# Optimization experiments

Hardware: AMD Instinct MI355X
Metric: run time of the kernel (lower is better)

Reference implementation:

```python
import jax, jax.numpy as jnp
import numpy as np

IN_CH = 128
OUT_CH = 1
N_NODES = 20000
N_EDGES = 640000
EPS = 1e-5


def setup_inputs() -> dict:
    key = jax.random.key(0)
    ks = jax.random.split(key, 8)
    x = jax.random.normal(ks[0], (N_NODES, IN_CH), dtype=jnp.float32)
    edge_index = jax.random.randint(ks[1], (2, N_EDGES), 0, N_NODES, dtype=jnp.int64)
    s1 = 1.0 / np.sqrt(2 * IN_CH)
    s2 = 1.0 / np.sqrt(IN_CH)
    return {
        "x": x,
        "edge_index": edge_index,
        "W1": jax.random.normal(ks[2], (2 * IN_CH, IN_CH), dtype=jnp.float32) * s1,
        "b1": jnp.zeros((IN_CH,), dtype=jnp.float32),
        "bn_g": jnp.ones((IN_CH,), dtype=jnp.float32),
        "bn_b": jnp.zeros((IN_CH,), dtype=jnp.float32),
        "W2": jax.random.normal(ks[3], (IN_CH, IN_CH), dtype=jnp.float32) * s2,
        "b2": jnp.zeros((IN_CH,), dtype=jnp.float32),
        "ln_g": jnp.ones((IN_CH,), dtype=jnp.float32),
        "ln_b": jnp.zeros((IN_CH,), dtype=jnp.float32),
        "W3": jax.random.normal(ks[4], (IN_CH, OUT_CH), dtype=jnp.float32) * s2,
        "b3": jnp.zeros((OUT_CH,), dtype=jnp.float32),
    }


def gcn_conv(h, src, dst, num_nodes, bias):
    # h: [num_nodes, F] already linearly transformed. GCN norm with self loops:
    # deg[i] = 1 + in-degree(i); norm_e = deg[src]^-1/2 * deg[dst]^-1/2
    deg = jnp.zeros((num_nodes,), h.dtype).at[dst].add(1.0) + 1.0
    dinv = deg ** -0.5
    norm = dinv[src] * dinv[dst]                      # [E]
    agg = jnp.zeros_like(h).at[dst].add(h[src] * norm[:, None])
    agg = agg + h * (dinv * dinv)[:, None]            # self-loop contribution
    return agg + bias


def reference(x, edge_index, W1, b1, bn_g, bn_b, W2, b2, ln_g, ln_b, W3, b3):
    src, dst = edge_index[0], edge_index[1]
    E = src.shape[0]
    # edge features: [E, 2*IN_CH]
    ef = jnp.concatenate([x[src], x[dst]], axis=1)
    # GCNConv 1 over E "nodes" (edge-feature rows)
    h = gcn_conv(ef @ W1, src, dst, E, b1)
    # BatchNorm1d (training-mode batch stats, biased variance)
    mean = h.mean(axis=0)
    var = h.var(axis=0)
    h = (h - mean) * jax.lax.rsqrt(var + EPS) * bn_g + bn_b
    h = jax.nn.relu(h)
    # GCNConv 2
    h = gcn_conv(h @ W2, src, dst, E, b2)
    # LayerNorm over feature dim
    mu = h.mean(axis=-1, keepdims=True)
    v = h.var(axis=-1, keepdims=True)
    h = (h - mu) * jax.lax.rsqrt(v + EPS) * ln_g + ln_b
    h = jax.nn.relu(h)
    out = h @ W3 + b3                                  # [E, 1]
    return out.squeeze()
```

## Files before the change

kernel.cpp:

```cpp
#include <hip/hip_runtime.h>
#include <hip/hip_bf16.h>

#define NN 20000
#define NE 640000
#define F  128
#define EPSN 1e-5f

typedef __bf16 bf16;
typedef bf16  bf16x8 __attribute__((ext_vector_type(8)));
typedef bf16  bf16x4 __attribute__((ext_vector_type(4)));
typedef bf16  bf16x2 __attribute__((ext_vector_type(2)));
typedef float f32x4  __attribute__((ext_vector_type(4)));
typedef float f32x2  __attribute__((ext_vector_type(2)));
typedef unsigned short u16;

__global__ void k_cvt_idx(const void* __restrict__ ei_raw, int* __restrict__ srcb,
                          int* __restrict__ dstb, int* __restrict__ cnt) {
  const int* e32 = (const int*)ei_raw;
  const long long* e64 = (const long long*)ei_raw;
  bool is64 = true;
#pragma unroll
  for (int k = 0; k < 8; ++k) is64 = is64 && (e32[2 * k + 1] == 0);
  int e = blockIdx.x * 256 + threadIdx.x;
  if (e < NE) {
    int s, d;
    if (is64) { s = (int)e64[e]; d = (int)e64[NE + e]; }
    else      { s = e32[e];      d = e32[NE + e]; }
    srcb[e] = s; dstb[e] = d;
    atomicAdd(&cnt[d], 1);
  }
}

__global__ __launch_bounds__(256) void k1_gemm1(const float* __restrict__ x,
        const float* __restrict__ W1, bf16* __restrict__ xa, bf16* __restrict__ xb) {
  __shared__ float XT[64][129];
  int row0 = blockIdx.x * 64;
  int half = blockIdx.y >> 1;
  int cb   = (blockIdx.y & 1) * 64;
  const float* W = W1 + (size_t)half * F * F;
  bf16* out = half ? xb : xa;
  int t = threadIdx.x;
#pragma unroll
  for (int i = 0; i < 8; ++i) {
    int flat = i * 1024 + t * 4;
    int r = flat >> 7, c = flat & 127;
    int gr = row0 + r;
    f32x4 v = {0.f, 0.f, 0.f, 0.f};
    if (gr < NN) v = *(const f32x4*)(x + (size_t)gr * F + c);
    XT[r][c] = v[0]; XT[r][c + 1] = v[1]; XT[r][c + 2] = v[2]; XT[r][c + 3] = v[3];
  }
  __syncthreads();
  int tc = t & 15, tr = t >> 4;
  float acc[4][4] = {};
  for (int k = 0; k < F; ++k) {
    f32x4 wv = *(const f32x4*)(W + (size_t)k * F + cb + tc * 4);
    float x0 = XT[tr * 4 + 0][k], x1 = XT[tr * 4 + 1][k];
    float x2 = XT[tr * 4 + 2][k], x3 = XT[tr * 4 + 3][k];
#pragma unroll
    for (int j = 0; j < 4; ++j) {
      acc[0][j] += x0 * wv[j]; acc[1][j] += x1 * wv[j];
      acc[2][j] += x2 * wv[j]; acc[3][j] += x3 * wv[j];
    }
  }
#pragma unroll
  for (int i = 0; i < 4; ++i) {
    int gr = row0 + tr * 4 + i;
    if (gr < NN) {
      bf16x4 o;
#pragma unroll
      for (int j = 0; j < 4; ++j) o[j] = (bf16)acc[i][j];
      *(bf16x4*)(out + (size_t)gr * F + cb + tc * 4) = o;
    }
  }
}

__global__ __launch_bounds__(1024) void k3_scan(const int* __restrict__ cnt,
        int* __restrict__ ptr, int* __restrict__ cursor,
        float* __restrict__ dinv, float* __restrict__ invdeg) {
  __shared__ int wsum[16];
  __shared__ int carry_s;
  int t = threadIdx.x;
  int lane = t & 63, wv = t >> 6;
  if (t == 0) carry_s = 0;
  __syncthreads();
  for (int c0 = 0; c0 < NN; c0 += 1024) {
    int i = c0 + t;
    int v = (i < NN) ? cnt[i] : 0;
    int s = v;
#pragma unroll
    for (int off = 1; off < 64; off <<= 1) {
      int n = __shfl_up(s, off);
      if (lane >= off) s += n;
    }
    if (lane == 63) wsum[wv] = s;
    __syncthreads();
    int carry = carry_s;
    int wbase = 0;
#pragma unroll
    for (int k2 = 0; k2 < 16; ++k2) wbase += (k2 < wv) ? wsum[k2] : 0;
    int incl = s + wbase;
    if (i < NN) {
      int excl = carry + incl - v;
      ptr[i] = excl; cursor[i] = excl;
      float deg = (float)(v + 1);
      dinv[i] = rsqrtf(deg);
      invdeg[i] = 1.0f / deg;
    }
    __syncthreads();
    if (t == 1023) carry_s = carry + incl;
    __syncthreads();
  }
  if (t == 0) ptr[NN] = carry_s;
}

__global__ void k4_hhead(const int* __restrict__ srcb, const int* __restrict__ dstb,
                         const bf16* __restrict__ xa, const bf16* __restrict__ xb,
                         bf16* __restrict__ hh) {
  int flat = blockIdx.x * 256 + threadIdx.x;
  int j = flat >> 4, ch = flat & 15;
  if (j >= NN) return;
  int s = srcb[j], d = dstb[j];
  bf16x8 a = *(const bf16x8*)(xa + (size_t)s * F + ch * 8);
  bf16x8 b = *(const bf16x8*)(xb + (size_t)d * F + ch * 8);
  bf16x8 o;
#pragma unroll
  for (int m = 0; m < 8; ++m) o[m] = (bf16)((float)a[m] + (float)b[m]);
  *(bf16x8*)(hh + (size_t)j * F + ch * 8) = o;
}

__global__ void k5_fill(const int* __restrict__ srcb, const int* __restrict__ dstb,
                        int* __restrict__ cursor, int* __restrict__ csr_s) {
  int e = blockIdx.x * 256 + threadIdx.x;
  if (e < NE) {
    int d = dstb[e];
    int pos = atomicAdd(&cursor[d], 1);
    csr_s[pos] = srcb[e];
  }
}

__global__ __launch_bounds__(256) void k6_conv1head(const int* __restrict__ ptr,
        const int* __restrict__ csr_s, const bf16* __restrict__ hh,
        const float* __restrict__ dinv, const float* __restrict__ invdeg,
        const float* __restrict__ b1, float* __restrict__ h1h) {
  int w = threadIdx.x >> 6, lane = threadIdx.x & 63;
  int i = blockIdx.x * 4 + w;
  int c2 = lane * 2;
  int beg = ptr[i], end = ptr[i + 1];
  float a0 = 0.f, a1 = 0.f;
  int q = beg;
  for (; q + 1 < end; q += 2) {
    int s0 = csr_s[q], s1 = csr_s[q + 1];
    float d0 = dinv[s0], d1 = dinv[s1];
    bf16x2 h0 = *(const bf16x2*)(hh + (size_t)s0 * F + c2);
    bf16x2 h1v = *(const bf16x2*)(hh + (size_t)s1 * F + c2);
    a0 += d0 * (float)h0[0] + d1 * (float)h1v[0];
    a1 += d0 * (float)h0[1] + d1 * (float)h1v[1];
  }
  if (q < end) {
    int s0 = csr_s[q];
    float d0 = dinv[s0];
    bf16x2 h0 = *(const bf16x2*)(hh + (size_t)s0 * F + c2);
    a0 += d0 * (float)h0[0]; a1 += d0 * (float)h0[1];
  }
  bf16x2 self = *(const bf16x2*)(hh + (size_t)i * F + c2);
  float di = dinv[i], iv = invdeg[i];
  f32x2 o = {di * a0 + (float)self[0] * iv + b1[c2],
             di * a1 + (float)self[1] * iv + b1[c2 + 1]};
  *(f32x2*)(h1h + (size_t)i * F + c2) = o;
}

__global__ __launch_bounds__(256) void k7_stats(const int* __restrict__ srcb,
        const int* __restrict__ dstb, const bf16* __restrict__ xa,
        const bf16* __restrict__ xb, const float* __restrict__ h1h,
        const float* __restrict__ b1, float* __restrict__ stats) {
  int w = threadIdx.x >> 6, lane = threadIdx.x & 63;
  int c2 = lane * 2;
  int base = blockIdx.x * 128;
  float bc0 = b1[c2], bc1 = b1[c2 + 1];
  float s0 = 0.f, s1 = 0.f, q0 = 0.f, q1 = 0.f;
  for (int r = w; r < 128; r += 4) {
    int e = base + r;
    float v0, v1;
    if (e < NN) {
      f32x2 hv = *(const f32x2*)(h1h + (size_t)e * F + c2);
      v0 = hv[0]; v1 = hv[1];
    } else {
      int se = srcb[e], de = dstb[e];
      bf16x2 av = *(const bf16x2*)(xa + (size_t)se * F + c2);
      bf16x2 bv = *(const bf16x2*)(xb + (size_t)de * F + c2);
      v0 = (float)av[0] + (float)bv[0] + bc0;
      v1 = (float)av[1] + (float)bv[1] + bc1;
    }
    s0 += v0; s1 += v1; q0 += v0 * v0; q1 += v1 * v1;
  }
  __shared__ float SS[4][128], QQ[4][128];
  SS[w][c2] = s0; SS[w][c2 + 1] = s1;
  QQ[w][c2] = q0; QQ[w][c2 + 1] = q1;
  __syncthreads();
  int t = threadIdx.x;
  if (t < 128) atomicAdd(&stats[t], SS[0][t] + SS[1][t] + SS[2][t] + SS[3][t]);
  else atomicAdd(&stats[t], QQ[0][t - 128] + QQ[1][t - 128] + QQ[2][t - 128] + QQ[3][t - 128]);
}

__global__ __launch_bounds__(256) void k8_final(const float* __restrict__ stats,
        const float* __restrict__ bn_g, const float* __restrict__ bn_b,
        const float* __restrict__ b1, const float* __restrict__ W2,
        float* __restrict__ P, float* __restrict__ Qh, float* __restrict__ Qt,
        u16* __restrict__ W2t) {
  int t = threadIdx.x;
  if (t < 128) {
    float mean = stats[t] * (1.0f / NE);
    float var = stats[128 + t] * (1.0f / NE) - mean * mean;
    float rs = rsqrtf(var + EPSN);
    float p = bn_g[t] * rs;
    float sh = bn_b[t] - mean * p;
    P[t] = p; Qh[t] = sh; Qt[t] = p * b1[t] + sh;
  }
  for (int i = 0; i < 64; ++i) {
    int flat = i * 256 + t;
    int k = flat >> 7, c = flat & 127;
    union { bf16 b; u16 u; } cv;
    cv.b = (bf16)W2[(size_t)k * F + c];
    W2t[(size_t)c * F + k] = cv.u;
  }
}

__global__ __launch_bounds__(256) void k9a_headgemm(const float* __restrict__ h1h,
        const float* __restrict__ P, const float* __restrict__ Qh,
        const u16* __restrict__ W2t, bf16* __restrict__ h2ph) {
  __shared__ __align__(16) bf16 A[64 * 128];
  __shared__ __align__(16) bf16 B[128 * 128];
  int t = threadIdx.x;
  int row0 = blockIdx.x * 64;
  const bf16x8* srcB = (const bf16x8*)W2t;
#pragma unroll
  for (int i = 0; i < 8; ++i) {
    int ch = i * 256 + t;
    int r = ch >> 4, cir = ch & 15;
    *(bf16x8*)&B[r * 128 + ((cir ^ (r & 7)) << 3)] = srcB[ch];
  }
  {
    int r = t >> 2, sub = t & 3;
    int gr = row0 + r;
#pragma unroll
    for (int j = 0; j < 4; ++j) {
      int c0 = sub * 32 + j * 8;
      f32x4 v0 = {0.f,0.f,0.f,0.f}, v1 = {0.f,0.f,0.f,0.f};
      if (gr < NN) {
        v0 = *(const f32x4*)(h1h + (size_t)gr * F + c0);
        v1 = *(const f32x4*)(h1h + (size_t)gr * F + c0 + 4);
      }
      f32x4 p0 = *(const f32x4*)(P + c0), p1 = *(const f32x4*)(P + c0 + 4);
      f32x4 q0 = *(const f32x4*)(Qh + c0), q1 = *(const f32x4*)(Qh + c0 + 4);
      bf16x8 o;
#pragma unroll
      for (int m = 0; m < 4; ++m) {
        o[m]     = (bf16)fmaxf(v0[m] * p0[m] + q0[m], 0.f);
        o[m + 4] = (bf16)fmaxf(v1[m] * p1[m] + q1[m], 0.f);
      }
      int ch = c0 >> 3;
      *(bf16x8*)&A[r * 128 + ((ch ^ (r & 7)) << 3)] = o;
    }
  }
  __syncthreads();
  int lane = t & 63, w = t >> 6;
  int lr = lane & 15, g = lane >> 4;
  int arow = w * 16 + lr;
  bf16x8 af[4];
#pragma unroll
  for (int kk = 0; kk < 4; ++kk)
    af[kk] = *(const bf16x8*)&A[arow * 128 + (((kk * 4 + g) ^ (arow & 7)) << 3)];
  f32x4 acc[8];
#pragma unroll
  for (int n = 0; n < 8; ++n) {
    f32x4 a = {0.f,0.f,0.f,0.f};
    int col = n * 16 + lr;
#pragma unroll
    for (int kk = 0; kk < 4; ++kk) {
      bf16x8 bfr = *(const bf16x8*)&B[col * 128 + (((kk * 4 + g) ^ (col & 7)) << 3)];
      a = __builtin_amdgcn_mfma_f32_16x16x32_bf16(af[kk], bfr, a, 0, 0, 0);
    }
    acc[n] = a;
  }
#pragma unroll
  for (int n = 0; n < 8; ++n) {
#pragma unroll
    for (int r4 = 0; r4 < 4; ++r4) {
      int gr = row0 + w * 16 + g * 4 + r4;
      if (gr < NN) h2ph[(size_t)gr * F + n * 16 + lr] = (bf16)acc[n][r4];
    }
  }
}

__global__ __launch_bounds__(256) void k9b_head(const int* __restrict__ ptr,
        const int* __restrict__ csr_s, const bf16* __restrict__ h2ph,
        const float* __restrict__ dinv, const float* __restrict__ invdeg,
        const float* __restrict__ b2, const float* __restrict__ lng,
        const float* __restrict__ lnb, const float* __restrict__ W3,
        const float* __restrict__ b3, float* __restrict__ out) {
  int w = threadIdx.x >> 6, lane = threadIdx.x & 63;
  int i = blockIdx.x * 4 + w;
  int c2 = lane * 2;
  int beg = ptr[i], end = ptr[i + 1];
  float a0 = 0.f, a1 = 0.f;
  int q = beg;
  for (; q + 1 < end; q += 2) {
    int s0 = csr_s[q], s1 = csr_s[q + 1];
    float d0 = dinv[s0], d1 = dinv[s1];
    bf16x2 h0 = *(const bf16x2*)(h2ph + (size_t)s0 * F + c2);
    bf16x2 h1v = *(const bf16x2*)(h2ph + (size_t)s1 * F + c2);
    a0 += d0 * (float)h0[0] + d1 * (float)h1v[0];
    a1 += d0 * (float)h0[1] + d1 * (float)h1v[1];
  }
  if (q < end) {
    int s0 = csr_s[q];
    float d0 = dinv[s0];
    bf16x2 h0 = *(const bf16x2*)(h2ph + (size_t)s0 * F + c2);
    a0 += d0 * (float)h0[0]; a1 += d0 * (float)h0[1];
  }
  bf16x2 self = *(const bf16x2*)(h2ph + (size_t)i * F + c2);
  float di = dinv[i], iv = invdeg[i];
  float h20 = di * a0 + (float)self[0] * iv + b2[c2];
  float h21 = di * a1 + (float)self[1] * iv + b2[c2 + 1];
  float s1v = h20 + h21, s2v = h20 * h20 + h21 * h21;
#pragma unroll
  for (int m = 1; m < 64; m <<= 1) { s1v += __shfl_xor(s1v, m); s2v += __shfl_xor(s2v, m); }
  float mean = s1v * (1.0f / F);
  float var = s2v * (1.0f / F) - mean * mean;
  float rs = rsqrtf(var + EPSN);
  float y = fmaxf((h20 - mean) * rs * lng[c2] + lnb[c2], 0.f) * W3[c2]
          + fmaxf((h21 - mean) * rs * lng[c2 + 1] + lnb[c2 + 1], 0.f) * W3[c2 + 1];
#pragma unroll
  for (int m = 1; m < 64; m <<= 1) y += __shfl_xor(y, m);
  if (lane == 0) out[i] = y + b3[0];
}

__global__ __launch_bounds__(256) void k9c_tail(const int* __restrict__ srcb,
        const int* __restrict__ dstb, const bf16* __restrict__ xa,
        const bf16* __restrict__ xb, const float* __restrict__ P,
        const float* __restrict__ Qt, const u16* __restrict__ W2t,
        const float* __restrict__ b2, const float* __restrict__ lng,
        const float* __restrict__ lnb, const float* __restrict__ W3,
        const float* __restrict__ b3, float* __restrict__ out) {
  __shared__ __align__(16) bf16 B[128 * 128];
  int t = threadIdx.x;
  int e0 = NN + blockIdx.x * 64;
  const bf16x8* srcB = (const bf16x8*)W2t;
#pragma unroll
  for (int i = 0; i < 8; ++i) {
    int ch = i * 256 + t;
    int r = ch >> 4, cir = ch & 15;
    *(bf16x8*)&B[r * 128 + ((cir ^ (r & 7)) << 3)] = srcB[ch];
  }
  int lane = t & 63, w = t >> 6;
  int lr = lane & 15, g = lane >> 4;
  int e = e0 + w * 16 + lr;
  bool ok = (e < NE);
  int se = 0, de = 0;
  if (ok) { se = srcb[e]; de = dstb[e]; }
  bf16x8 af[4];
#pragma unroll
  for (int kk = 0; kk < 4; ++kk) {
    int c0 = kk * 32 + g * 8;
    bf16x8 o;
    if (ok) {
      bf16x8 av = *(const bf16x8*)(xa + (size_t)se * F + c0);
      bf16x8 bv = *(const bf16x8*)(xb + (size_t)de * F + c0);
      f32x4 p0 = *(const f32x4*)(P + c0), p1 = *(const f32x4*)(P + c0 + 4);
      f32x4 q0 = *(const f32x4*)(Qt + c0), q1 = *(const f32x4*)(Qt + c0 + 4);
#pragma unroll
      for (int m = 0; m < 4; ++m) {
        o[m]     = (bf16)fmaxf(((float)av[m] + (float)bv[m]) * p0[m] + q0[m], 0.f);
        o[m + 4] = (bf16)fmaxf(((float)av[m + 4] + (float)bv[m + 4]) * p1[m] + q1[m], 0.f);
      }
    } else {
#pragma unroll
      for (int m = 0; m < 8; ++m) o[m] = (bf16)0.f;
    }
    af[kk] = o;
  }
  __syncthreads();
  f32x4 acc[8];
#pragma unroll
  for (int n = 0; n < 8; ++n) {
    f32x4 a = {0.f,0.f,0.f,0.f};
    int col = n * 16 + lr;
#pragma unroll
    for (int kk = 0; kk < 4; ++kk) {
      bf16x8 bfr = *(const bf16x8*)&B[col * 128 + (((kk * 4 + g) ^ (col & 7)) << 3)];
      a = __builtin_amdgcn_mfma_f32_16x16x32_bf16(af[kk], bfr, a, 0, 0, 0);
    }
    acc[n] = a;
  }
  float b2v[8], lgv[8], lbv[8], w3v[8];
#pragma unroll
  for (int n = 0; n < 8; ++n) {
    int cc = n * 16 + lr;
    b2v[n] = b2[cc]; lgv[n] = lng[cc]; lbv[n] = lnb[cc]; w3v[n] = W3[cc];
  }
  float b3v = b3[0];
#pragma unroll
  for (int r4 = 0; r4 < 4; ++r4) {
    float vv[8];
    float s = 0.f, q = 0.f;
#pragma unroll
    for (int n = 0; n < 8; ++n) {
      float v = acc[n][r4] + b2v[n];
      vv[n] = v; s += v; q += v * v;
    }
#pragma unroll
    for (int m = 1; m < 16; m <<= 1) { s += __shfl_xor(s, m); q += __shfl_xor(q, m); }
    float mean = s * (1.0f / F);
    float var = q * (1.0f / F) - mean * mean;
    float rs = rsqrtf(var + EPSN);
    float o = 0.f;
#pragma unroll
    for (int n = 0; n < 8; ++n)
      o += fmaxf((vv[n] - mean) * rs * lgv[n] + lbv[n], 0.f) * w3v[n];
#pragma unroll
    for (int m = 1; m < 16; m <<= 1) o += __shfl_xor(o, m);
    int eo = e0 + w * 16 + g * 4 + r4;
    if (lr == 0 && eo < NE) out[eo] = o + b3v;
  }
}

extern "C" void kernel_launch(void* const* d_in, const int* in_sizes, int n_in,
                              void* d_out, int out_size, void* d_ws, size_t ws_size,
                              hipStream_t stream) {
  const float* x   = (const float*)d_in[0];
  const void*  ei  = d_in[1];
  const float* W1  = (const float*)d_in[2];
  const float* b1  = (const float*)d_in[3];
  const float* bng = (const float*)d_in[4];
  const float* bnb = (const float*)d_in[5];
  const float* W2  = (const float*)d_in[6];
  const float* b2  = (const float*)d_in[7];
  const float* lng = (const float*)d_in[8];
  const float* lnb = (const float*)d_in[9];
  const float* W3  = (const float*)d_in[10];
  const float* b3  = (const float*)d_in[11];
  float* out = (float*)d_out;

  char* ws = (char*)d_ws;
  size_t off = 0;
  auto alloc = [&](size_t bytes) -> char* {
    off = (off + 511) & ~(size_t)511;
    char* p = ws + off;
    off += bytes;
    return p;
  };
  const size_t NFh = (size_t)NN * F * 2;
  bf16*  xa     = (bf16*)alloc(NFh);
  bf16*  xb     = (bf16*)alloc(NFh);
  bf16*  hh     = (bf16*)alloc(NFh);
  float* h1h    = (float*)alloc((size_t)NN * F * 4);
  int*   srcb   = (int*)alloc((size_t)NE * 4);
  int*   dstb   = (int*)alloc((size_t)NE * 4);
  int*   csr_s  = (int*)alloc((size_t)NE * 4);
  int*   cnt    = (int*)alloc((size_t)NN * 4);
  int*   ptrb   = (int*)alloc((size_t)(NN + 1) * 4);
  int*   cursor = (int*)alloc((size_t)NN * 4);
  float* dinv   = (float*)alloc((size_t)NN * 4);
  float* invdeg = (float*)alloc((size_t)NN * 4);
  float* stats  = (float*)alloc(256 * 4);
  float* Pp     = (float*)alloc(128 * 4);
  float* Qh     = (float*)alloc(128 * 4);
  float* Qt     = (float*)alloc(128 * 4);
  u16*   W2t    = (u16*)alloc((size_t)F * F * 2);
  bf16*  h2ph   = hh;

  hipMemsetAsync(cnt, 0, (size_t)NN * 4, stream);
  hipMemsetAsync(stats, 0, 256 * 4, stream);

  k_cvt_idx<<<2500, 256, 0, stream>>>(ei, srcb, dstb, cnt);
  k1_gemm1<<<dim3(313, 4), 256, 0, stream>>>(x, W1, xa, xb);
  k3_scan<<<1, 1024, 0, stream>>>(cnt, ptrb, cursor, dinv, invdeg);
  k4_hhead<<<1250, 256, 0, stream>>>(srcb, dstb, xa, xb, hh);
  k5_fill<<<2500, 256, 0, stream>>>(srcb, dstb, cursor, csr_s);
  k6_conv1head<<<5000, 256, 0, stream>>>(ptrb, csr_s, hh, dinv, invdeg, b1, h1h);
  k7_stats<<<5000, 256, 0, stream>>>(srcb, dstb, xa, xb, h1h, b1, stats);
  k8_final<<<1, 256, 0, stream>>>(stats, bng, bnb, b1, W2, Pp, Qh, Qt, W2t);
  k9a_headgemm<<<313, 256, 0, stream>>>(h1h, Pp, Qh, W2t, h2ph);
  k9b_head<<<5000, 256, 0, stream>>>(ptrb, csr_s, h2ph, dinv, invdeg, b2, lng, lnb, W3, b3, out);
  k9c_tail<<<9688, 256, 0, stream>>>(srcb, dstb, xa, xb, Pp, Qt, W2t, b2, lng, lnb, W3, b3, out);
}
```

Before: 547.9 us.

## Compute BatchNorm statistics algebraically from per-node counts and fuse cross terms into conv1

Rather than gathering xa[src]+xb[dst] for all 620k tail edges to accumulate batch statistics, the tail sum and sum-of-squares are expanded algebraically. Per-node source and destination counts weight the squared node rows, and the cross term sum(xa[s]*xb[d]) is gathered per destination inside the conv1 kernel using flagged CSR entries. The conv gathers switch to 8-wide bf16 vector loads spread over four lane groups. The tail GEMM kernel now processes four row chunks per block so the W2 tile in LDS is loaded once per chunk set. This adds more atomics in the index conversion, an extra NN×F float buffer, and packs a flag into bit 16 of the CSR source index, which assumes node ids fit in 16 bits.

After: 464.7 us. -15.2%, faster.

```diff
diff --git a/kernel.cpp b/kernel.cpp
--- a/kernel.cpp
+++ b/kernel.cpp
@@ -3,19 +3,20 @@
 
 #define NN 20000
 #define NE 640000
+#define TAILN (NE - NN)
 #define F  128
 #define EPSN 1e-5f
 
 typedef __bf16 bf16;
 typedef bf16  bf16x8 __attribute__((ext_vector_type(8)));
 typedef bf16  bf16x4 __attribute__((ext_vector_type(4)));
-typedef bf16  bf16x2 __attribute__((ext_vector_type(2)));
 typedef float f32x4  __attribute__((ext_vector_type(4)));
 typedef float f32x2  __attribute__((ext_vector_type(2)));
 typedef unsigned short u16;
 
 __global__ void k_cvt_idx(const void* __restrict__ ei_raw, int* __restrict__ srcb,
-                          int* __restrict__ dstb, int* __restrict__ cnt) {
+                          int* __restrict__ dstb, int* __restrict__ cnt,
+                          int* __restrict__ cst, int* __restrict__ cdt) {
   const int* e32 = (const int*)ei_raw;
   const long long* e64 = (const long long*)ei_raw;
   bool is64 = true;
@@ -28,6 +29,7 @@
     else      { s = e32[e];      d = e32[NE + e]; }
     srcb[e] = s; dstb[e] = d;
     atomicAdd(&cnt[d], 1);
+    if (e >= NN) { atomicAdd(&cst[s], 1); atomicAdd(&cdt[d], 1); }
   }
 }
 
@@ -134,87 +136,164 @@
   if (e < NE) {
     int d = dstb[e];
     int pos = atomicAdd(&cursor[d], 1);
-    csr_s[pos] = srcb[e];
-  }
-}
-
-__global__ __launch_bounds__(256) void k6_conv1head(const int* __restrict__ ptr,
+    csr_s[pos] = srcb[e] | ((e >= NN) ? (1 << 16) : 0);
+  }
+}
+
+__global__ __launch_bounds__(256) void k6_conv1cross(const int* __restrict__ ptr,
         const int* __restrict__ csr_s, const bf16* __restrict__ hh,
+        const bf16* __restrict__ xa, const bf16* __restrict__ xb,
         const float* __restrict__ dinv, const float* __restrict__ invdeg,
-        const float* __restrict__ b1, float* __restrict__ h1h) {
+        const float* __restrict__ b1, float* __restrict__ h1h,
+        float* __restrict__ crossrow) {
   int w = threadIdx.x >> 6, lane = threadIdx.x & 63;
+  int g = lane >> 4, k = lane & 15;
   int i = blockIdx.x * 4 + w;
-  int c2 = lane * 2;
+  int c0 = k * 8;
   int beg = ptr[i], end = ptr[i + 1];
-  float a0 = 0.f, a1 = 0.f;
-  int q = beg;
-  for (; q + 1 < end; q += 2) {
-    int s0 = csr_s[q], s1 = csr_s[q + 1];
+  float acc[8] = {0,0,0,0,0,0,0,0}, z[8] = {0,0,0,0,0,0,0,0};
+  int q = beg + g;
+  for (; q + 4 < end; q += 8) {
+    int v0 = csr_s[q], v1 = csr_s[q + 4];
+    int s0 = v0 & 0xFFFF, s1 = v1 & 0xFFFF;
+    float f0 = (v0 >> 16) ? 1.f : 0.f, f1 = (v1 >> 16) ? 1.f : 0.f;
     float d0 = dinv[s0], d1 = dinv[s1];
-    bf16x2 h0 = *(const bf16x2*)(hh + (size_t)s0 * F + c2);
-    bf16x2 h1v = *(const bf16x2*)(hh + (size_t)s1 * F + c2);
-    a0 += d0 * (float)h0[0] + d1 * (float)h1v[0];
-    a1 += d0 * (float)h0[1] + d1 * (float)h1v[1];
+    bf16x8 h0 = *(const bf16x8*)(hh + (size_t)s0 * F + c0);
+    bf16x8 x0 = *(const bf16x8*)(xa + (size_t)s0 * F + c0);
+    bf16x8 h1 = *(const bf16x8*)(hh + (size_t)s1 * F + c0);
+    bf16x8 x1 = *(const bf16x8*)(xa + (size_t)s1 * F + c0);
+#pragma unroll
+    for (int j = 0; j < 8; ++j) {
+      acc[j] += d0 * (float)h0[j] + d1 * (float)h1[j];
+      z[j]   += f0 * (float)x0[j] + f1 * (float)x1[j];
+    }
   }
   if (q < end) {
-    int s0 = csr_s[q];
+    int v0 = csr_s[q];
+    int s0 = v0 & 0xFFFF;
+    float f0 = (v0 >> 16) ? 1.f : 0.f;
     float d0 = dinv[s0];
-    bf16x2 h0 = *(const bf16x2*)(hh + (size_t)s0 * F + c2);
-    a0 += d0 * (float)h0[0]; a1 += d0 * (float)h0[1];
-  }
-  bf16x2 self = *(const bf16x2*)(hh + (size_t)i * F + c2);
-  float di = dinv[i], iv = invdeg[i];
-  f32x2 o = {di * a0 + (float)self[0] * iv + b1[c2],
-             di * a1 + (float)self[1] * iv + b1[c2 + 1]};
-  *(f32x2*)(h1h + (size_t)i * F + c2) = o;
-}
-
-__global__ __launch_bounds__(256) void k7_stats(const int* __restrict__ srcb,
-        const int* __restrict__ dstb, const bf16* __restrict__ xa,
-        const bf16* __restrict__ xb, const float* __restrict__ h1h,
-        const float* __restrict__ b1, float* __restrict__ stats) {
-  int w = threadIdx.x >> 6, lane = threadIdx.x & 63;
-  int c2 = lane * 2;
-  int base = blockIdx.x * 128;
-  float bc0 = b1[c2], bc1 = b1[c2 + 1];
-  float s0 = 0.f, s1 = 0.f, q0 = 0.f, q1 = 0.f;
-  for (int r = w; r < 128; r += 4) {
-    int e = base + r;
-    float v0, v1;
-    if (e < NN) {
-      f32x2 hv = *(const f32x2*)(h1h + (size_t)e * F + c2);
-      v0 = hv[0]; v1 = hv[1];
-    } else {
-      int se = srcb[e], de = dstb[e];
-      bf16x2 av = *(const bf16x2*)(xa + (size_t)se * F + c2);
-      bf16x2 bv = *(const bf16x2*)(xb + (size_t)de * F + c2);
-      v0 = (float)av[0] + (float)bv[0] + bc0;
-      v1 = (float)av[1] + (float)bv[1] + bc1;
-    }
-    s0 += v0; s1 += v1; q0 += v0 * v0; q1 += v1 * v1;
-  }
-  __shared__ float SS[4][128], QQ[4][128];
-  SS[w][c2] = s0; SS[w][c2 + 1] = s1;
-  QQ[w][c2] = q0; QQ[w][c2 + 1] = q1;
+    bf16x8 h0 = *(const bf16x8*)(hh + (size_t)s0 * F + c0);
+    bf16x8 x0 = *(const bf16x8*)(xa + (size_t)s0 * F + c0);
+#pragma unroll
+    for (int j = 0; j < 8; ++j) {
+      acc[j] += d0 * (float)h0[j];
+      z[j]   += f0 * (float)x0[j];
+    }
+  }
+#pragma unroll
+  for (int m = 16; m < 64; m <<= 1) {
+#pragma unroll
+    for (int j = 0; j < 8; ++j) {
+      acc[j] += __shfl_xor(acc[j], m);
+      z[j]   += __shfl_xor(z[j], m);
+    }
+  }
+  if (g == 0) {
+    float di = dinv[i], iv = invdeg[i];
+    bf16x8 self = *(const bf16x8*)(hh + (size_t)i * F + c0);
+    f32x4 bA = *(const f32x4*)(b1 + c0), bB = *(const f32x4*)(b1 + c0 + 4);
+    f32x4 o0, o1;
+#pragma unroll
+    for (int j = 0; j < 4; ++j) {
+      o0[j] = di * acc[j]     + (float)self[j]     * iv + bA[j];
+      o1[j] = di * acc[j + 4] + (float)self[j + 4] * iv + bB[j];
+    }
+    *(f32x4*)(h1h + (size_t)i * F + c0) = o0;
+    *(f32x4*)(h1h + (size_t)i * F + c0 + 4) = o1;
+  } else if (g == 1) {
+    bf16x8 xbv = *(const bf16x8*)(xb + (size_t)i * F + c0);
+    f32x4 o0, o1;
+#pragma unroll
+    for (int j = 0; j < 4; ++j) {
+      o0[j] = (float)xbv[j]     * z[j];
+      o1[j] = (float)xbv[j + 4] * z[j + 4];
+    }
+    *(f32x4*)(crossrow + (size_t)i * F + c0) = o0;
+    *(f32x4*)(crossrow + (size_t)i * F + c0 + 4) = o1;
+  }
+}
+
+__global__ __launch_bounds__(256) void k7sr(const float* __restrict__ h1h,
+        const float* __restrict__ crossrow, const bf16* __restrict__ xa,
+        const bf16* __restrict__ xb, const int* __restrict__ cst,
+        const int* __restrict__ cdt, float* __restrict__ statsB) {
+  int t = threadIdx.x;
+  int w = t >> 6, lane = t & 63, k = lane & 15;
+  int rg = t >> 4;
+  int c0 = k * 8;
+  int base = blockIdx.x * 200;
+  float A1[8] = {0,0,0,0,0,0,0,0}, A2[8] = {0,0,0,0,0,0,0,0};
+  float B1[8] = {0,0,0,0,0,0,0,0}, B2[8] = {0,0,0,0,0,0,0,0};
+  float Cc[8] = {0,0,0,0,0,0,0,0};
+  for (int r = rg; r < 200; r += 16) {
+    int n = base + r;
+    f32x4 h0 = *(const f32x4*)(h1h + (size_t)n * F + c0);
+    f32x4 h1 = *(const f32x4*)(h1h + (size_t)n * F + c0 + 4);
+    f32x4 cr0 = *(const f32x4*)(crossrow + (size_t)n * F + c0);
+    f32x4 cr1 = *(const f32x4*)(crossrow + (size_t)n * F + c0 + 4);
+    bf16x8 av = *(const bf16x8*)(xa + (size_t)n * F + c0);
+    bf16x8 bv = *(const bf16x8*)(xb + (size_t)n * F + c0);
+    float ca = (float)cst[n], cb = (float)cdt[n];
+#pragma unroll
+    for (int j = 0; j < 4; ++j) {
+      A1[j] += h0[j]; A2[j] += h0[j] * h0[j];
+      A1[j + 4] += h1[j]; A2[j + 4] += h1[j] * h1[j];
+      Cc[j] += cr0[j]; Cc[j + 4] += cr1[j];
+    }
+#pragma unroll
+    for (int j = 0; j < 8; ++j) {
+      float a = (float)av[j], b = (float)bv[j];
+      B1[j] += ca * a + cb * b;
+      B2[j] += ca * a * a + cb * b * b;
+    }
+  }
+#pragma unroll
+  for (int m = 16; m < 64; m <<= 1) {
+#pragma unroll
+    for (int j = 0; j < 8; ++j) {
+      A1[j] += __shfl_xor(A1[j], m); A2[j] += __shfl_xor(A2[j], m);
+      B1[j] += __shfl_xor(B1[j], m); B2[j] += __shfl_xor(B2[j], m);
+      Cc[j] += __shfl_xor(Cc[j], m);
+    }
+  }
+  __shared__ float L[4][5][128];
+  if (lane < 16) {
+#pragma unroll
+    for (int j = 0; j < 8; ++j) {
+      L[w][0][c0 + j] = A1[j]; L[w][1][c0 + j] = A2[j];
+      L[w][2][c0 + j] = B1[j]; L[w][3][c0 + j] = B2[j];
+      L[w][4][c0 + j] = Cc[j];
+    }
+  }
   __syncthreads();
-  int t = threadIdx.x;
-  if (t < 128) atomicAdd(&stats[t], SS[0][t] + SS[1][t] + SS[2][t] + SS[3][t]);
-  else atomicAdd(&stats[t], QQ[0][t - 128] + QQ[1][t - 128] + QQ[2][t - 128] + QQ[3][t - 128]);
-}
-
-__global__ __launch_bounds__(256) void k8_final(const float* __restrict__ stats,
+  if (t < 128) {
+#pragma unroll
+    for (int term = 0; term < 5; ++term) {
+      float v = L[0][term][t] + L[1][term][t] + L[2][term][t] + L[3][term][t];
+      atomicAdd(&statsB[term * 128 + t], v);
+    }
+  }
+}
+
+__global__ __launch_bounds__(256) void k8_final(const float* __restrict__ statsB,
         const float* __restrict__ bn_g, const float* __restrict__ bn_b,
         const float* __restrict__ b1, const float* __restrict__ W2,
         float* __restrict__ P, float* __restrict__ Qh, float* __restrict__ Qt,
         u16* __restrict__ W2t) {
   int t = threadIdx.x;
   if (t < 128) {
-    float mean = stats[t] * (1.0f / NE);
-    float var = stats[128 + t] * (1.0f / NE) - mean * mean;
+    float A1 = statsB[t], A2 = statsB[128 + t], B1v = statsB[256 + t];
+    float B2v = statsB[384 + t], Cv = statsB[512 + t];
+    float b1c = b1[t];
+    float S = A1 + B1v + (float)TAILN * b1c;
+    float Q = A2 + B2v + 2.f * Cv + 2.f * b1c * B1v + (float)TAILN * b1c * b1c;
+    float mean = S * (1.0f / NE);
+    float var = Q * (1.0f / NE) - mean * mean;
     float rs = rsqrtf(var + EPSN);
     float p = bn_g[t] * rs;
     float sh = bn_b[t] - mean * p;
-    P[t] = p; Qh[t] = sh; Qt[t] = p * b1[t] + sh;
+    P[t] = p; Qh[t] = sh; Qt[t] = p * b1c + sh;
   }
   for (int i = 0; i < 64; ++i) {
     int flat = i * 256 + t;
@@ -299,39 +378,61 @@
         const float* __restrict__ lnb, const float* __restrict__ W3,
         const float* __restrict__ b3, float* __restrict__ out) {
   int w = threadIdx.x >> 6, lane = threadIdx.x & 63;
+  int g = lane >> 4, k = lane & 15;
   int i = blockIdx.x * 4 + w;
-  int c2 = lane * 2;
+  int c0 = k * 8;
   int beg = ptr[i], end = ptr[i + 1];
-  float a0 = 0.f, a1 = 0.f;
-  int q = beg;
-  for (; q + 1 < end; q += 2) {
-    int s0 = csr_s[q], s1 = csr_s[q + 1];
+  float acc[8] = {0,0,0,0,0,0,0,0};
+  int q = beg + g;
+  for (; q + 4 < end; q += 8) {
+    int s0 = csr_s[q] & 0xFFFF, s1 = csr_s[q + 4] & 0xFFFF;
     float d0 = dinv[s0], d1 = dinv[s1];
-    bf16x2 h0 = *(const bf16x2*)(h2ph + (size_t)s0 * F + c2);
-    bf16x2 h1v = *(const bf16x2*)(h2ph + (size_t)s1 * F + c2);
-    a0 += d0 * (float)h0[0] + d1 * (float)h1v[0];
-    a1 += d0 * (float)h0[1] + d1 * (float)h1v[1];
+    bf16x8 h0 = *(const bf16x8*)(h2ph + (size_t)s0 * F + c0);
+    bf16x8 h1 = *(const bf16x8*)(h2ph + (size_t)s1 * F + c0);
+#pragma unroll
+    for (int j = 0; j < 8; ++j)
+      acc[j] += d0 * (float)h0[j] + d1 * (float)h1[j];
   }
   if (q < end) {
-    int s0 = csr_s[q];
+    int s0 = csr_s[q] & 0xFFFF;
     float d0 = dinv[s0];
-    bf16x2 h0 = *(const bf16x2*)(h2ph + (size_t)s0 * F + c2);
-    a0 += d0 * (float)h0[0]; a1 += d0 * (float)h0[1];
-  }
-  bf16x2 self = *(const bf16x2*)(h2ph + (size_t)i * F + c2);
+    bf16x8 h0 = *(const bf16x8*)(h2ph + (size_t)s0 * F + c0);
+#pragma unroll
+    for (int j = 0; j < 8; ++j) acc[j] += d0 * (float)h0[j];
+  }
+#pragma unroll
+  for (int m = 16; m < 64; m <<= 1) {
+#pragma unroll
+    for (int j = 0; j < 8; ++j) acc[j] += __shfl_xor(acc[j], m);
+  }
   float di = dinv[i], iv = invdeg[i];
-  float h20 = di * a0 + (float)self[0] * iv + b2[c2];
-  float h21 = di * a1 + (float)self[1] * iv + b2[c2 + 1];
-  float s1v = h20 + h21, s2v = h20 * h20 + h21 * h21;
-#pragma unroll
-  for (int m = 1; m < 64; m <<= 1) { s1v += __shfl_xor(s1v, m); s2v += __shfl_xor(s2v, m); }
+  bf16x8 self = *(const bf16x8*)(h2ph + (size_t)i * F + c0);
+  f32x4 b2A = *(const f32x4*)(b2 + c0), b2B = *(const f32x4*)(b2 + c0 + 4);
+  float h2[8];
+#pragma unroll
+  for (int j = 0; j < 4; ++j) {
+    h2[j]     = di * acc[j]     + (float)self[j]     * iv + b2A[j];
+    h2[j + 4] = di * acc[j + 4] + (float)self[j + 4] * iv + b2B[j];
+  }
+  float s1v = 0.f, s2v = 0.f;
+#pragma unroll
+  for (int j = 0; j < 8; ++j) { s1v += h2[j]; s2v += h2[j] * h2[j]; }
+#pragma unroll
+  for (int m = 1; m < 16; m <<= 1) { s1v += __shfl_xor(s1v, m); s2v += __shfl_xor(s2v, m); }
   float mean = s1v * (1.0f / F);
   float var = s2v * (1.0f / F) - mean * mean;
   float rs = rsqrtf(var + EPSN);
-  float y = fmaxf((h20 - mean) * rs * lng[c2] + lnb[c2], 0.f) * W3[c2]
-          + fmaxf((h21 - mean) * rs * lng[c2 + 1] + lnb[c2 + 1], 0.f) * W3[c2 + 1];
-#pragma unroll
-  for (int m = 1; m < 64; m <<= 1) y += __shfl_xor(y, m);
+  f32x4 lgA = *(const f32x4*)(lng + c0), lgB = *(const f32x4*)(lng + c0 + 4);
+  f32x4 lbA = *(const f32x4*)(lnb + c0), lbB = *(const f32x4*)(lnb + c0 + 4);
+  f32x4 w3A = *(const f32x4*)(W3 + c0),  w3B = *(const f32x4*)(W3 + c0 + 4);
+  float y = 0.f;
+#pragma unroll
+  for (int j = 0; j < 4; ++j) {
+    y += fmaxf((h2[j]     - mean) * rs * lgA[j] + lbA[j], 0.f) * w3A[j];
+    y += fmaxf((h2[j + 4] - mean) * rs * lgB[j] + lbB[j], 0.f) * w3B[j];
+  }
+#pragma unroll
+  for (int m = 1; m < 16; m <<= 1) y += __shfl_xor(y, m);
   if (lane == 0) out[i] = y + b3[0];
 }
 
@@ -344,7 +445,6 @@
         const float* __restrict__ b3, float* __restrict__ out) {
   __shared__ __align__(16) bf16 B[128 * 128];
   int t = threadIdx.x;
-  int e0 = NN + blockIdx.x * 64;
   const bf16x8* srcB = (const bf16x8*)W2t;
 #pragma unroll
   for (int i = 0; i < 8; ++i) {
@@ -352,46 +452,10 @@
     int r = ch >> 4, cir = ch & 15;
     *(bf16x8*)&B[r * 128 + ((cir ^ (r & 7)) << 3)] = srcB[ch];
   }
+  __syncthreads();
   int lane = t & 63, w = t >> 6;
   int lr = lane & 15, g = lane >> 4;
-  int e = e0 + w * 16 + lr;
-  bool ok = (e < NE);
-  int se = 0, de = 0;
-  if (ok) { se = srcb[e]; de = dstb[e]; }
-  bf16x8 af[4];
-#pragma unroll
-  for (int kk = 0; kk < 4; ++kk) {
-    int c0 = kk * 32 + g * 8;
-    bf16x8 o;
-    if (ok) {
-      bf16x8 av = *(const bf16x8*)(xa + (size_t)se * F + c0);
-      bf16x8 bv = *(const bf16x8*)(xb + (size_t)de * F + c0);
-      f32x4 p0 = *(const f32x4*)(P + c0), p1 = *(const f32x4*)(P + c0 + 4);
-      f32x4 q0 = *(const f32x4*)(Qt + c0), q1 = *(const f32x4*)(Qt + c0 + 4);
-#pragma unroll
-      for (int m = 0; m < 4; ++m) {
-        o[m]     = (bf16)fmaxf(((float)av[m] + (float)bv[m]) * p0[m] + q0[m], 0.f);
-        o[m + 4] = (bf16)fmaxf(((float)av[m + 4] + (float)bv[m + 4]) * p1[m] + q1[m], 0.f);
-      }
-    } else {
-#pragma unroll
-      for (int m = 0; m < 8; ++m) o[m] = (bf16)0.f;
-    }
-    af[kk] = o;
-  }
-  __syncthreads();
-  f32x4 acc[8];
-#pragma unroll
-  for (int n = 0; n < 8; ++n) {
-    f32x4 a = {0.f,0.f,0.f,0.f};
-    int col = n * 16 + lr;
-#pragma unroll
-    for (int kk = 0; kk < 4; ++kk) {
-      bf16x8 bfr = *(const bf16x8*)&B[col * 128 + (((kk * 4 + g) ^ (col & 7)) << 3)];
-      a = __builtin_amdgcn_mfma_f32_16x16x32_bf16(af[kk], bfr, a, 0, 0, 0);
-    }
-    acc[n] = a;
-  }
+  int ebase = NN + blockIdx.x * 256 + w * 64;
   float b2v[8], lgv[8], lbv[8], w3v[8];
 #pragma unroll
   for (int n = 0; n < 8; ++n) {
@@ -399,28 +463,67 @@
     b2v[n] = b2[cc]; lgv[n] = lng[cc]; lbv[n] = lnb[cc]; w3v[n] = W3[cc];
   }
   float b3v = b3[0];
-#pragma unroll
-  for (int r4 = 0; r4 < 4; ++r4) {
-    float vv[8];
-    float s = 0.f, q = 0.f;
+  for (int rc = 0; rc < 4; ++rc) {
+    int e = ebase + rc * 16 + lr;
+    bool ok = (e < NE);
+    int se = 0, de = 0;
+    if (ok) { se = srcb[e]; de = dstb[e]; }
+    bf16x8 af[4];
+#pragma unroll
+    for (int kk = 0; kk < 4; ++kk) {
+      int c0 = kk * 32 + g * 8;
+      bf16x8 o;
+      if (ok) {
+        bf16x8 av = *(const bf16x8*)(xa + (size_t)se * F + c0);
+        bf16x8 bv = *(const bf16x8*)(xb + (size_t)de * F + c0);
+        f32x4 p0 = *(const f32x4*)(P + c0), p1 = *(const f32x4*)(P + c0 + 4);
+        f32x4 q0 = *(const f32x4*)(Qt + c0), q1 = *(const f32x4*)(Qt + c0 + 4);
+#pragma unroll
+        for (int m = 0; m < 4; ++m) {
+          o[m]     = (bf16)fmaxf(((float)av[m] + (float)bv[m]) * p0[m] + q0[m], 0.f);
+          o[m + 4] = (bf16)fmaxf(((float)av[m + 4] + (float)bv[m + 4]) * p1[m] + q1[m], 0.f);
+        }
+      } else {
+#pragma unroll
+        for (int m = 0; m < 8; ++m) o[m] = (bf16)0.f;
+      }
+      af[kk] = o;
+    }
+    f32x4 acc[8];
 #pragma unroll
     for (int n = 0; n < 8; ++n) {
-      float v = acc[n][r4] + b2v[n];
-      vv[n] = v; s += v; q += v * v;
-    }
-#pragma unroll
-    for (int m = 1; m < 16; m <<= 1) { s += __shfl_xor(s, m); q += __shfl_xor(q, m); }
-    float mean = s * (1.0f / F);
-    float var = q * (1.0f / F) - mean * mean;
-    float rs = rsqrtf(var + EPSN);
-    float o = 0.f;
-#pragma unroll
-    for (int n = 0; n < 8; ++n)
-      o += fmaxf((vv[n] - mean) * rs * lgv[n] + lbv[n], 0.f) * w3v[n];
-#pragma unroll
-    for (int m = 1; m < 16; m <<= 1) o += __shfl_xor(o, m);
-    int eo = e0 + w * 16 + g * 4 + r4;
-    if (lr == 0 && eo < NE) out[eo] = o + b3v;
+      f32x4 a = {0.f,0.f,0.f,0.f};
+      int col = n * 16 + lr;
+#pragma unroll
+      for (int kk = 0; kk < 4; ++kk) {
+        bf16x8 bfr = *(const bf16x8*)&B[col * 128 + (((kk * 4 + g) ^ (col & 7)) << 3)];
+        a = __builtin_amdgcn_mfma_f32_16x16x32_bf16(af[kk], bfr, a, 0, 0, 0);
+      }
+      acc[n] = a;
+    }
+#pragma unroll
+    for (int r4 = 0; r4 < 4; ++r4) {
+      float vv[8];
+      float s = 0.f, q = 0.f;
+#pragma unroll
+      for (int n = 0; n < 8; ++n) {
+        float v = acc[n][r4] + b2v[n];
+        vv[n] = v; s += v; q += v * v;
+      }
+#pragma unroll
+      for (int m = 1; m < 16; m <<= 1) { s += __shfl_xor(s, m); q += __shfl_xor(q, m); }
+      float mean = s * (1.0f / F);
+      float var = q * (1.0f / F) - mean * mean;
+      float rs = rsqrtf(var + EPSN);
+      float o = 0.f;
+#pragma unroll
+      for (int n = 0; n < 8; ++n)
+        o += fmaxf((vv[n] - mean) * rs * lgv[n] + lbv[n], 0.f) * w3v[n];
+#pragma unroll
+      for (int m = 1; m < 16; m <<= 1) o += __shfl_xor(o, m);
+      int eo = ebase + rc * 16 + g * 4 + r4;
+      if (lr == 0 && eo < NE) out[eo] = o + b3v;
+    }
   }
 }
 
@@ -454,15 +557,18 @@
   bf16*  xb     = (bf16*)alloc(NFh);
   bf16*  hh     = (bf16*)alloc(NFh);
   float* h1h    = (float*)alloc((size_t)NN * F * 4);
+  float* crossr = (float*)alloc((size_t)NN * F * 4);
   int*   srcb   = (int*)alloc((size_t)NE * 4);
   int*   dstb   = (int*)alloc((size_t)NE * 4);
   int*   csr_s  = (int*)alloc((size_t)NE * 4);
   int*   cnt    = (int*)alloc((size_t)NN * 4);
+  int*   cst    = (int*)alloc((size_t)NN * 4);
+  int*   cdt    = (int*)alloc((size_t)NN * 4);
   int*   ptrb   = (int*)alloc((size_t)(NN + 1) * 4);
   int*   cursor = (int*)alloc((size_t)NN * 4);
   float* dinv   = (float*)alloc((size_t)NN * 4);
   float* invdeg = (float*)alloc((size_t)NN * 4);
-  float* stats  = (float*)alloc(256 * 4);
+  float* statsB = (float*)alloc(5 * 128 * 4);
   float* Pp     = (float*)alloc(128 * 4);
   float* Qh     = (float*)alloc(128 * 4);
   float* Qt     = (float*)alloc(128 * 4);
@@ -470,17 +576,22 @@
   bf16*  h2ph   = hh;
 
   hipMemsetAsync(cnt, 0, (size_t)NN * 4, stream);
-  hipMemsetAsync(stats, 0, 256 * 4, stream);
-
-  k_cvt_idx<<<2500, 256, 0, stream>>>(ei, srcb, dstb, cnt);
+  hipMemsetAsync(cst, 0, (size_t)NN * 4, stream);
+  hipMemsetAsync(cdt, 0, (size_t)NN * 4, stream);
+  hipMemsetAsync(statsB, 0, 5 * 128 * 4, stream);
+
+  k_cvt_idx<<<2500, 256, 0, stream>>>(ei, srcb, dstb, cnt, cst, cdt);
   k1_gemm1<<<dim3(313, 4), 256, 0, stream>>>(x, W1, xa, xb);
   k3_scan<<<1, 1024, 0, stream>>>(cnt, ptrb, cursor, dinv, invdeg);
   k4_hhead<<<1250, 256, 0, stream>>>(srcb, dstb, xa, xb, hh);
   k5_fill<<<2500, 256, 0, stream>>>(srcb, dstb, cursor, csr_s);
-  k6_conv1head<<<5000, 256, 0, stream>>>(ptrb, csr_s, hh, dinv, invdeg, b1, h1h);
-  k7_stats<<<5000, 256, 0, stream>>>(srcb, dstb, xa, xb, h1h, b1, stats);
-  k8_final<<<1, 256, 0, stream>>>(stats, bng, bnb, b1, W2, Pp, Qh, Qt, W2t);
+  k6_conv1cross<<<5000, 256, 0, stream>>>(ptrb, csr_s, hh, xa, xb, dinv, invdeg, b1,
+                                          h1h, crossr);
+  k7sr<<<100, 256, 0, stream>>>(h1h, crossr, xa, xb, cst, cdt, statsB);
+  k8_final<<<1, 256, 0, stream>>>(statsB, bng, bnb, b1, W2, Pp, Qh, Qt, W2t);
   k9a_headgemm<<<313, 256, 0, stream>>>(h1h, Pp, Qh, W2t, h2ph);
-  k9b_head<<<5000, 256, 0, stream>>>(ptrb, csr_s, h2ph, dinv, invdeg, b2, lng, lnb, W3, b3, out);
-  k9c_tail<<<9688, 256, 0, stream>>>(srcb, dstb, xa, xb, Pp, Qt, W2t, b2, lng, lnb, W3, b3, out);
-}
+  k9b_head<<<5000, 256, 0, stream>>>(ptrb, csr_s, h2ph, dinv, invdeg, b2, lng, lnb,
+                                     W3, b3, out);
+  k9c_tail<<<2422, 256, 0, stream>>>(srcb, dstb, xa, xb, Pp, Qt, W2t, b2, lng, lnb,
+                                     W3, b3, out);
+}
```
